# Performance work log

Hardware: AMD Instinct MI355X
Metric: run time of the kernel (lower is better)

Reference implementation:

```python
import jax, jax.numpy as jnp
import numpy as np

HIDDEN = 1024
NUM_HEADS = 16
HEAD_DIM = HIDDEN // NUM_HEADS  # 64
ROPE_DIM = HEAD_DIM // 2        # 32 (per-axis rotary dim)
EPS = 1e-6


def _make_rope_tables(dim, grid_h, grid_w, theta=10000.0):
    # pt_seq_len == ft_seq_len, so t_h = arange(H), t_w = arange(W)
    freqs = 1.0 / theta ** (np.arange(0, dim, 2, dtype=np.float32)[: dim // 2] / dim)  # [dim//2]
    fh = np.repeat(np.outer(np.arange(grid_h, dtype=np.float32), freqs), 2, axis=-1)  # [H, dim]
    fw = np.repeat(np.outer(np.arange(grid_w, dtype=np.float32), freqs), 2, axis=-1)  # [W, dim]
    fh = np.broadcast_to(fh[:, None, :], (grid_h, grid_w, dim))
    fw = np.broadcast_to(fw[None, :, :], (grid_h, grid_w, dim))
    f2d = np.concatenate([fh, fw], axis=-1).reshape(grid_h * grid_w, 2 * dim)  # [HW, 2*dim]
    return jnp.asarray(np.cos(f2d)), jnp.asarray(np.sin(f2d))


def _rms_norm(x, w, eps=EPS):
    var = jnp.mean(jnp.square(x), axis=-1, keepdims=True)
    return x * jax.lax.rsqrt(var + eps) * w


def _rotate_half(x):
    x1 = x[..., 0::2]
    x2 = x[..., 1::2]
    return jnp.stack([-x2, x1], axis=-1).reshape(x.shape)


def _apply_rope(x, cos, sin):
    # x: [B, H, S, D]; cos/sin: [S, D]
    return x * cos + _rotate_half(x) * sin


def setup_inputs() -> dict:
    key = jax.random.key(0)
    ks = jax.random.split(key, 12)
    B, IMG_H, IMG_W, CND_H, CND_W = 2, 64, 64, 32, 32
    img_len, cnd_len = IMG_H * IMG_W, CND_H * CND_W
    xav = (6.0 / (HIDDEN + HIDDEN)) ** 0.5
    inp = {
        'image_tokens': jax.random.normal(ks[0], (B, img_len, HIDDEN), jnp.float32),
        'condition_tokens': jax.random.normal(ks[1], (B, cnd_len, HIDDEN), jnp.float32),
        'q_norm_w': jnp.ones((HIDDEN,), jnp.float32),
        'kv_norm_w': jnp.ones((HIDDEN,), jnp.float32),
        'q_head_norm_w': jnp.ones((HEAD_DIM,), jnp.float32),
        'k_head_norm_w': jnp.ones((HEAD_DIM,), jnp.float32),
        'q_w': jax.random.uniform(ks[2], (HIDDEN, HIDDEN), jnp.float32, -xav, xav),
        'q_b': jnp.zeros((HIDDEN,), jnp.float32),
        'k_w': jax.random.uniform(ks[3], (HIDDEN, HIDDEN), jnp.float32, -xav, xav),
        'k_b': jnp.zeros((HIDDEN,), jnp.float32),
        'v_w': jax.random.uniform(ks[4], (HIDDEN, HIDDEN), jnp.float32, -xav, xav),
        'v_b': jnp.zeros((HIDDEN,), jnp.float32),
        'o_w': jax.random.uniform(ks[5], (HIDDEN, HIDDEN), jnp.float32, -xav, xav),
        'o_b': jnp.zeros((HIDDEN,), jnp.float32),
        'alpha': jnp.full((1,), 0.5, jnp.float32),  # nonzero so backward exercises the attn path
    }
    ic, isn = _make_rope_tables(ROPE_DIM, IMG_H, IMG_W)
    cc, cs = _make_rope_tables(ROPE_DIM, CND_H, CND_W)
    inp.update(image_cos=ic, image_sin=isn, cond_cos=cc, cond_sin=cs)
    return inp


def reference(image_tokens, condition_tokens, q_norm_w, kv_norm_w, q_head_norm_w,
              k_head_norm_w, q_w, q_b, k_w, k_b, v_w, v_b, o_w, o_b, alpha,
              image_cos, image_sin, cond_cos, cond_sin):
    B, Li, _ = image_tokens.shape
    Lc = condition_tokens.shape[1]
    qn = _rms_norm(image_tokens, q_norm_w)
    kvn = _rms_norm(condition_tokens, kv_norm_w)
    # projections (torch Linear: x @ W.T + b); weights here stored [out, in]
    q = (qn @ q_w.T + q_b).reshape(B, Li, NUM_HEADS, HEAD_DIM).transpose(0, 2, 1, 3)
    k = (kvn @ k_w.T + k_b).reshape(B, Lc, NUM_HEADS, HEAD_DIM).transpose(0, 2, 1, 3)
    v = (kvn @ v_w.T + v_b).reshape(B, Lc, NUM_HEADS, HEAD_DIM).transpose(0, 2, 1, 3)
    q = _rms_norm(q, q_head_norm_w)
    k = _rms_norm(k, k_head_norm_w)
    q = _apply_rope(q, image_cos, image_sin)
    k = _apply_rope(k, cond_cos, cond_sin)
    scale = 1.0 / jnp.sqrt(jnp.asarray(HEAD_DIM, q.dtype))
    scores = jnp.einsum('bhqd,bhkd->bhqk', q, k) * scale
    attn = jax.nn.softmax(scores, axis=-1)
    out = jnp.einsum('bhqk,bhkd->bhqd', attn, v)
    out = out.transpose(0, 2, 1, 3).reshape(B, Li, HIDDEN)
    update = out @ o_w.T + o_b
    return image_tokens + alpha.reshape(1, 1, 1) * update
```

## Files before the change

kernel.cpp:

```cpp
#include <hip/hip_runtime.h>

typedef __bf16 bf16x8 __attribute__((ext_vector_type(8)));
typedef __bf16 bf16x4 __attribute__((ext_vector_type(4)));
typedef float  f32x4  __attribute__((ext_vector_type(4)));
typedef float  f32x16 __attribute__((ext_vector_type(16)));
typedef unsigned u32x2 __attribute__((ext_vector_type(2)));

#define DEVINL __device__ __forceinline__

DEVINL void gload_lds16(const void* g, void* l) {
  __builtin_amdgcn_global_load_lds((const __attribute__((address_space(1))) void*)g,
                                   (__attribute__((address_space(3))) void*)l, 16, 0, 0);
}

DEVINL unsigned pkbf(float a, float b) {
  union { __bf16 h[2]; unsigned u; } c;
  c.h[0] = (__bf16)a; c.h[1] = (__bf16)b;
  return c.u;
}

DEVINL float fast_exp2(float x) {
#if __has_builtin(__builtin_amdgcn_exp2f)
  return __builtin_amdgcn_exp2f(x);
#else
  float r;
  asm volatile("v_exp_f32 %0, %1" : "=v"(r) : "v"(x));
  return r;
#endif
}

DEVINL float2 swap32(float x) {
  u32x2 r = __builtin_amdgcn_permlane32_swap(__float_as_uint(x), __float_as_uint(x), false, false);
  return make_float2(__uint_as_float(r.x), __uint_as_float(r.y));
}

__global__ __launch_bounds__(256) void prep_kernel(
    const float* __restrict__ XA, const float* __restrict__ WA, __bf16* __restrict__ YA,
    const float* __restrict__ XB, const float* __restrict__ WB, __bf16* __restrict__ YB,
    const float* __restrict__ wq, const float* __restrict__ wk,
    const float* __restrict__ wv, const float* __restrict__ wo,
    __bf16* __restrict__ oq, __bf16* __restrict__ ok,
    __bf16* __restrict__ ov, __bf16* __restrict__ oo) {
  int rb = blockIdx.x, tid = threadIdx.x;
  if (rb < 10240) {
    const float* X; const float* W; __bf16* Y; int row;
    if (rb < 8192) { X = XA; W = WA; Y = YA; row = rb; }
    else { X = XB; W = WB; Y = YB; row = rb - 8192; }
    const float4* xr = (const float4*)(X + (size_t)row * 1024);
    float4 v = xr[tid];
    float ss = v.x * v.x + v.y * v.y + v.z * v.z + v.w * v.w;
#pragma unroll
    for (int m = 1; m < 64; m <<= 1) ss += __shfl_xor(ss, m);
    __shared__ float part[4];
    if ((tid & 63) == 0) part[tid >> 6] = ss;
    __syncthreads();
    float tot = part[0] + part[1] + part[2] + part[3];
    float rn = rsqrtf(tot * (1.0f / 1024.0f) + 1e-6f);
    float4 wv4 = ((const float4*)W)[tid];
    bf16x4 y;
    y[0] = (__bf16)(v.x * rn * wv4.x);
    y[1] = (__bf16)(v.y * rn * wv4.y);
    y[2] = (__bf16)(v.z * rn * wv4.z);
    y[3] = (__bf16)(v.w * rn * wv4.w);
    *(bf16x4*)(Y + (size_t)row * 1024 + tid * 4) = y;
  } else {
    int gid = (rb - 10240) * 256 + tid;
    int which = gid >> 17;
    size_t off = (size_t)(gid & 131071) * 8;
    const float* s = (which == 0) ? wq : (which == 1) ? wk : (which == 2) ? wv : wo;
    __bf16* o = (which == 0) ? oq : (which == 1) ? ok : (which == 2) ? ov : oo;
    float4 v0 = *(const float4*)(s + off), v1 = *(const float4*)(s + off + 4);
    bf16x8 y;
    y[0] = (__bf16)v0.x; y[1] = (__bf16)v0.y; y[2] = (__bf16)v0.z; y[3] = (__bf16)v0.w;
    y[4] = (__bf16)v1.x; y[5] = (__bf16)v1.y; y[6] = (__bf16)v1.z; y[7] = (__bf16)v1.w;
    *(bf16x8*)(o + off) = y;
  }
}

template <typename EPIF>
DEVINL void gemm_core(const __bf16* __restrict__ A, const __bf16* __restrict__ Bw,
                      int m0, int n0, char* AsB, char* BsB, EPIF epi) {
  int tid = threadIdx.x, lane = tid & 63, w = tid >> 6, wr = w >> 1, wc = w & 1;
  f32x4 z4 = {0.f, 0.f, 0.f, 0.f};
  f32x4 acc[4][4];
#pragma unroll
  for (int i = 0; i < 4; i++)
#pragma unroll
    for (int j = 0; j < 4; j++) acc[i][j] = z4;

  auto STAGE = [&](int k0, int bsel) {
#pragma unroll
    for (int i = 0; i < 2; i++) {
      int chunk = i * 256 + tid;
      int row = chunk >> 2, cc = chunk & 3;
      gload_lds16(A + (size_t)(m0 + row) * 1024 + k0 + cc * 8,
                  AsB + bsel * 8192 + i * 4096 + w * 1024);
      gload_lds16(Bw + (size_t)(n0 + row) * 1024 + k0 + cc * 8,
                  BsB + bsel * 8192 + i * 4096 + w * 1024);
    }
  };

  STAGE(0, 0);
  int b = 0;
  for (int it = 0; it < 32; ++it) {
    if (it < 31) {
      STAGE((it + 1) * 32, b ^ 1);
      asm volatile("s_waitcnt vmcnt(4)" ::: "memory");
    } else {
      asm volatile("s_waitcnt vmcnt(0)" ::: "memory");
    }
    __builtin_amdgcn_s_barrier();
    asm volatile("" ::: "memory");
    const char* As = AsB + b * 8192;
    const char* Bs = BsB + b * 8192;
    bf16x8 af[4], bfr[4];
#pragma unroll
    for (int m = 0; m < 4; m++) {
      int r = wr * 64 + m * 16 + (lane & 15);
      af[m] = *(const bf16x8*)(As + r * 64 + ((lane >> 4) << 4));
    }
#pragma unroll
    for (int n = 0; n < 4; n++) {
      int r = wc * 64 + n * 16 + (lane & 15);
      bfr[n] = *(const bf16x8*)(Bs + r * 64 + ((lane >> 4) << 4));
    }
    __builtin_amdgcn_s_setprio(1);
#pragma unroll
    for (int m = 0; m < 4; m++)
#pragma unroll
      for (int n = 0; n < 4; n++)
        acc[m][n] = __builtin_amdgcn_mfma_f32_16x16x32_bf16(af[m], bfr[n], acc[m][n], 0, 0, 0);
    __builtin_amdgcn_s_setprio(0);
    __builtin_amdgcn_s_barrier();
    asm volatile("" ::: "memory");
    b ^= 1;
  }
  epi(acc, lane, wr, wc);
}

__global__ __launch_bounds__(256) void qkv_gemm_kernel(
    const __bf16* __restrict__ qn, const __bf16* __restrict__ kvn,
    const __bf16* __restrict__ wq, const __bf16* __restrict__ wkv,
    const float* __restrict__ qb, const float* __restrict__ kb, const float* __restrict__ vb,
    __bf16* __restrict__ Qt, __bf16* __restrict__ Kt, __bf16* __restrict__ Vt0) {
  __shared__ __attribute__((aligned(16))) char AsB[2 * 8192];
  __shared__ __attribute__((aligned(16))) char BsB[2 * 8192];
  int id = blockIdx.x;
  const __bf16 *A, *Bw; const float* bias; __bf16* Cout;
  int m0, n0, nloc;
  if (id < 512) {
    A = qn; Bw = wq; m0 = (id & 63) * 128; n0 = (id >> 6) * 128; nloc = n0;
    bias = qb; Cout = Qt;
  } else {
    int i2 = id - 512;
    A = kvn; Bw = wkv; m0 = (i2 & 15) * 128; n0 = (i2 >> 4) * 128;
    if (n0 < 1024) { bias = kb; Cout = Kt; nloc = n0; }
    else { bias = vb; Cout = Vt0; nloc = n0 - 1024; }
  }
  gemm_core(A, Bw, m0, n0, AsB, BsB,
            [&](f32x4 (&acc)[4][4], int lane, int wr, int wc) {
#pragma unroll
              for (int m = 0; m < 4; m++)
#pragma unroll
                for (int n = 0; n < 4; n++) {
                  int col = nloc + wc * 64 + n * 16 + (lane & 15);
                  float bv = bias[col];
#pragma unroll
                  for (int r = 0; r < 4; r++) {
                    int row = m0 + wr * 64 + m * 16 + ((lane >> 4) << 2) + r;
                    Cout[((size_t)row << 10) + col] = (__bf16)(acc[m][n][r] + bv);
                  }
                }
            });
}

__global__ __launch_bounds__(256) void gemm_o_kernel(
    const __bf16* __restrict__ A, const __bf16* __restrict__ Bw,
    const float* __restrict__ bias, float* __restrict__ Cout,
    const float* __restrict__ resid, const float* __restrict__ alphap) {
  __shared__ __attribute__((aligned(16))) char AsB[2 * 8192];
  __shared__ __attribute__((aligned(16))) char BsB[2 * 8192];
  int m0 = blockIdx.x * 128, n0 = blockIdx.y * 128;
  float aval = alphap[0];
  gemm_core(A, Bw, m0, n0, AsB, BsB,
            [&](f32x4 (&acc)[4][4], int lane, int wr, int wc) {
#pragma unroll
              for (int m = 0; m < 4; m++)
#pragma unroll
                for (int n = 0; n < 4; n++) {
                  int col = n0 + wc * 64 + n * 16 + (lane & 15);
                  float bv = bias[col];
#pragma unroll
                  for (int r = 0; r < 4; r++) {
                    int row = m0 + wr * 64 + m * 16 + ((lane >> 4) << 2) + r;
                    size_t idx = ((size_t)row << 10) + col;
                    Cout[idx] = resid[idx] + aval * (acc[m][n][r] + bv);
                  }
                }
            });
}

__global__ __launch_bounds__(256) void kprep_kernel(
    const __bf16* __restrict__ Kt, const float* __restrict__ KHW,
    const float* __restrict__ CCOS, const float* __restrict__ CSIN,
    __bf16* __restrict__ Kr,
    const __bf16* __restrict__ V, __bf16* __restrict__ Vt) {
  int rb = blockIdx.x, tid = threadIdx.x;
  if (rb < 1024) {
    int inst = rb * 32 + (tid >> 3);
    int sub = tid & 7;
    int token = inst >> 4, h = inst & 15;
    int b = token >> 10, pos = token & 1023;
    const __bf16* xp = Kt + ((size_t)token << 10) + h * 64 + sub * 8;
    bf16x8 xv = *(const bf16x8*)xp;
    float xf[8];
#pragma unroll
    for (int i = 0; i < 8; i++) xf[i] = (float)xv[i];
    float ss = 0.f;
#pragma unroll
    for (int i = 0; i < 8; i++) ss += xf[i] * xf[i];
    ss += __shfl_xor(ss, 1);
    ss += __shfl_xor(ss, 2);
    ss += __shfl_xor(ss, 4);
    float rn = rsqrtf(ss * (1.0f / 64.0f) + 1e-6f);
    const float* hwp = KHW + sub * 8;
    const float* cp = CCOS + ((size_t)pos << 6) + sub * 8;
    const float* sp = CSIN + ((size_t)pos << 6) + sub * 8;
    float xn[8], o[8];
#pragma unroll
    for (int i = 0; i < 8; i++) xn[i] = xf[i] * rn * hwp[i];
#pragma unroll
    for (int i = 0; i < 8; i += 2) {
      o[i] = xn[i] * cp[i] - xn[i + 1] * sp[i];
      o[i + 1] = xn[i + 1] * cp[i + 1] + xn[i] * sp[i + 1];
    }
    bf16x8 yv;
#pragma unroll
    for (int i = 0; i < 8; i++) yv[i] = (__bf16)o[i];
    *(bf16x8*)(Kr + (((size_t)((b << 4) + h) << 10) + pos) * 64 + sub * 8) = yv;
  } else {
    int bx = rb - 1024;
    int bh = bx >> 4;
    int j0 = (bx & 15) * 64;
    int b = bh >> 4, h = bh & 15;
#pragma unroll
    for (int it = 0; it < 2; ++it) {
      int c = it * 256 + tid;
      int jl = c >> 3, d0 = (c & 7) * 8;
      bf16x8 v = *(const bf16x8*)(V + (size_t)(b * 1024 + j0 + jl) * 1024 + h * 64 + d0);
#pragma unroll
      for (int i = 0; i < 8; i++)
        Vt[((size_t)bh * 64 + d0 + i) * 1024 + j0 + jl] = v[i];
    }
  }
}

__global__ __launch_bounds__(256, 3) void attn_kernel(
    const __bf16* __restrict__ Qt, const float* __restrict__ QHW,
    const float* __restrict__ QCOS, const float* __restrict__ QSIN,
    const __bf16* __restrict__ Kr, const __bf16* __restrict__ Vtr,
    __bf16* __restrict__ AO) {
  int tid = threadIdx.x, lane = tid & 63, w = tid >> 6;
  int lq = lane & 31, hi = lane >> 5;
  int wgid = blockIdx.x;
  int nid = (wgid & 7) * 128 + (wgid >> 3);
  int q0 = (nid & 31) * 128;
  int bh = nid >> 5, b = bh >> 4, h = bh & 15;
  const float QSC = 0.125f * 1.44269504088896340736f;

  __shared__ __attribute__((aligned(16))) __bf16 Ks[2][4096];
  __shared__ __attribute__((aligned(16))) __bf16 Vs[2][4096];

  const __bf16* Kbh = Kr + ((size_t)bh << 16);
  const __bf16* Vbh = Vtr + ((size_t)bh << 16);

  auto STAGE = [&](int T, int BSEL) {
#pragma unroll
    for (int i = 0; i < 2; i++) {
      int s = 2 * w + i;
      int kt = s >> 2, ds2 = s & 3;
      gload_lds16(Kbh + (size_t)(T * 64 + kt * 32 + lq) * 64 + ds2 * 16 + hi * 8,
                  (char*)Ks[BSEL] + s * 1024);
      int f = s >> 1, dh = s & 1;
      gload_lds16(Vbh + (size_t)(dh * 32 + lq) * 1024 + T * 64 + f * 16 + hi * 8,
                  (char*)Vs[BSEL] + s * 1024);
    }
  };

  STAGE(0, 0);

  bf16x8 qf[4];
  {
    int pos = q0 + w * 32 + lq;
    const __bf16* qp = Qt + ((size_t)(b * 4096 + pos) << 10) + h * 64 + hi * 8;
    float xf[4][8];
    float ss = 0.f;
#pragma unroll
    for (int ds = 0; ds < 4; ds++) {
      bf16x8 xv = *(const bf16x8*)(qp + ds * 16);
#pragma unroll
      for (int j = 0; j < 8; j++) { float f = (float)xv[j]; xf[ds][j] = f; ss += f * f; }
    }
    float2 sw = swap32(ss);
    float rn = rsqrtf((sw.x + sw.y) * (1.0f / 64.0f) + 1e-6f);
#pragma unroll
    for (int ds = 0; ds < 4; ds++) {
      int d0 = ds * 16 + hi * 8;
      const float* wp = QHW + d0;
      const float* cp = QCOS + ((size_t)pos << 6) + d0;
      const float* sp = QSIN + ((size_t)pos << 6) + d0;
      float4 wa = *(const float4*)wp, wb = *(const float4*)(wp + 4);
      float4 ca = *(const float4*)cp, cb = *(const float4*)(cp + 4);
      float4 sa = *(const float4*)sp, sb = *(const float4*)(sp + 4);
      float wv[8] = {wa.x, wa.y, wa.z, wa.w, wb.x, wb.y, wb.z, wb.w};
      float cv[8] = {ca.x, ca.y, ca.z, ca.w, cb.x, cb.y, cb.z, cb.w};
      float sv[8] = {sa.x, sa.y, sa.z, sa.w, sb.x, sb.y, sb.z, sb.w};
      float xn[8];
#pragma unroll
      for (int j = 0; j < 8; j++) xn[j] = xf[ds][j] * rn * wv[j];
      bf16x8 q8;
#pragma unroll
      for (int j = 0; j < 8; j += 2) {
        q8[j]     = (__bf16)((xn[j] * cv[j] - xn[j + 1] * sv[j]) * QSC);
        q8[j + 1] = (__bf16)((xn[j + 1] * cv[j + 1] + xn[j] * sv[j + 1]) * QSC);
      }
      qf[ds] = q8;
    }
  }

  f32x16 Z16;
#pragma unroll
  for (int r = 0; r < 16; r++) Z16[r] = 0.f;
  f32x16 accO[2];
  accO[0] = Z16; accO[1] = Z16;
  float srun = 0.f;

  int buf = 0;
  for (int t = 0; t < 16; t++) {
    if (t < 15) {
      STAGE(t + 1, buf ^ 1);
      asm volatile("s_waitcnt vmcnt(4)" ::: "memory");
    } else {
      asm volatile("s_waitcnt vmcnt(0)" ::: "memory");
    }
    __builtin_amdgcn_s_barrier();
    asm volatile("" ::: "memory");

    const char* kbase = (const char*)Ks[buf];
    const char* vbase = (const char*)Vs[buf];
    int loff = lane * 16;

    bf16x8 kf[8];
#pragma unroll
    for (int s = 0; s < 8; s++) kf[s] = *(const bf16x8*)(kbase + s * 1024 + loff);

    f32x16 accS[2];
    __builtin_amdgcn_s_setprio(1);
#pragma unroll
    for (int kt = 0; kt < 2; kt++) {
      accS[kt] = __builtin_amdgcn_mfma_f32_32x32x16_bf16(kf[kt * 4], qf[0], Z16, 0, 0, 0);
#pragma unroll
      for (int ds = 1; ds < 4; ds++)
        accS[kt] = __builtin_amdgcn_mfma_f32_32x32x16_bf16(kf[kt * 4 + ds], qf[ds], accS[kt], 0, 0, 0);
    }
    __builtin_amdgcn_s_setprio(0);

    float ssum = 0.f;
#pragma unroll
    for (int kt = 0; kt < 2; kt++)
#pragma unroll
      for (int r = 0; r < 16; r++) {
        float e = fast_exp2(accS[kt][r]);
        accS[kt][r] = e;
        ssum += e;
      }
    float2 sws = swap32(ssum);
    srun += sws.x + sws.y;

    unsigned pa[4][4];
#pragma unroll
    for (int kt = 0; kt < 2; kt++)
#pragma unroll
      for (int s2 = 0; s2 < 2; s2++) {
        int f = kt * 2 + s2, rb = s2 * 8;
        unsigned u  = pkbf(accS[kt][rb + 0], accS[kt][rb + 1]);
        unsigned v2 = pkbf(accS[kt][rb + 2], accS[kt][rb + 3]);
        unsigned w2 = pkbf(accS[kt][rb + 4], accS[kt][rb + 5]);
        unsigned x2 = pkbf(accS[kt][rb + 6], accS[kt][rb + 7]);
        u32x2 r02 = __builtin_amdgcn_permlane32_swap(u, w2, false, false);
        u32x2 r13 = __builtin_amdgcn_permlane32_swap(v2, x2, false, false);
        pa[f][0] = r02.x; pa[f][1] = r13.x; pa[f][2] = r02.y; pa[f][3] = r13.y;
      }

    bf16x8 vf[8];
#pragma unroll
    for (int s = 0; s < 8; s++) vf[s] = *(const bf16x8*)(vbase + s * 1024 + loff);

    __builtin_amdgcn_s_setprio(1);
#pragma unroll
    for (int f = 0; f < 4; f++) {
      union { unsigned u[4]; bf16x8 v; } pf;
      pf.u[0] = pa[f][0]; pf.u[1] = pa[f][1]; pf.u[2] = pa[f][2]; pf.u[3] = pa[f][3];
#pragma unroll
      for (int dh = 0; dh < 2; dh++)
        accO[dh] = __builtin_amdgcn_mfma_f32_32x32x16_bf16(pf.v, vf[f * 2 + dh], accO[dh], 0, 0, 0);
    }
    __builtin_amdgcn_s_setprio(0);

    __builtin_amdgcn_s_barrier();
    asm volatile("" ::: "memory");
    buf ^= 1;
  }

  __bf16* aobase = AO + (((size_t)b * 4096) << 10) + h * 64;
  float rinv = 1.0f / srun;
  int ri = __float_as_int(rinv);
#pragma unroll
  for (int r = 0; r < 16; r++) {
    int cr = (r & 3) + ((r >> 2) << 3) + (hi << 2);
    float rv = __int_as_float(__builtin_amdgcn_ds_bpermute(cr << 2, ri));
    size_t rowoff = ((size_t)(q0 + w * 32 + cr) << 10);
#pragma unroll
    for (int dh = 0; dh < 2; dh++)
      aobase[rowoff + dh * 32 + lq] = (__bf16)(accO[dh][r] * rv);
  }
}

extern "C" void kernel_launch(void* const* d_in, const int* in_sizes, int n_in,
                              void* d_out, int out_size, void* d_ws, size_t ws_size,
                              hipStream_t stream) {
  const float* img  = (const float*)d_in[0];
  const float* cnd  = (const float*)d_in[1];
  const float* qnw  = (const float*)d_in[2];
  const float* kvnw = (const float*)d_in[3];
  const float* qhw  = (const float*)d_in[4];
  const float* khw  = (const float*)d_in[5];
  const float* qw   = (const float*)d_in[6];
  const float* qb   = (const float*)d_in[7];
  const float* kw   = (const float*)d_in[8];
  const float* kb   = (const float*)d_in[9];
  const float* vw   = (const float*)d_in[10];
  const float* vb   = (const float*)d_in[11];
  const float* ow   = (const float*)d_in[12];
  const float* ob   = (const float*)d_in[13];
  const float* alpha= (const float*)d_in[14];
  const float* icos = (const float*)d_in[15];
  const float* isin = (const float*)d_in[16];
  const float* ccos = (const float*)d_in[17];
  const float* csin = (const float*)d_in[18];
  float* out = (float*)d_out;

  __bf16* p = (__bf16*)d_ws;
  __bf16* wqb = p; p += 1048576;
  __bf16* wkb = p; p += 1048576;
  __bf16* wvb = p; p += 1048576;
  __bf16* wob = p; p += 1048576;
  __bf16* qn  = p; p += 8388608;
  __bf16* kvn = p; p += 2097152;
  __bf16* Qt  = p; p += 8388608;
  __bf16* Kt  = p; p += 2097152;
  __bf16* Vt0 = p; p += 2097152;
  __bf16* Kr  = p; p += 2097152;
  __bf16* Vtr = p; p += 2097152;
  __bf16* AO  = qn;

  prep_kernel<<<12288, 256, 0, stream>>>(img, qnw, qn, cnd, kvnw, kvn,
                                         qw, kw, vw, ow, wqb, wkb, wvb, wob);

  qkv_gemm_kernel<<<768, 256, 0, stream>>>(qn, kvn, wqb, wkb, qb, kb, vb, Qt, Kt, Vt0);

  kprep_kernel<<<1536, 256, 0, stream>>>(Kt, khw, ccos, csin, Kr, Vt0, Vtr);

  attn_kernel<<<1024, 256, 0, stream>>>(Qt, qhw, icos, isin, Kr, Vtr, AO);

  gemm_o_kernel<<<dim3(64, 8), 256, 0, stream>>>(AO, wob, ob, out, img, alpha);
}
```

Baseline: 152.0 us.

## Split QK tiles into halves to cut registers and raise attention occupancy

Raises the attention kernel's launch bound from 3 to 4 waves per SIMD. The QK^T compute now runs in two 32-key halves that reuse one accumulator, so the exp/pack of one half overlaps with the MFMAs of the next and fewer registers are live at once. Staging addresses are precomputed once outside the loop, which removes per-iteration address arithmetic. The tighter register budget could cause spills, and the compiler's reordering may not give the intended overlap.

```diff
diff --git a/kernel.cpp b/kernel.cpp
--- a/kernel.cpp
+++ b/kernel.cpp
@@ -255,7 +255,7 @@
   }
 }
 
-__global__ __launch_bounds__(256, 3) void attn_kernel(
+__global__ __launch_bounds__(256, 4) void attn_kernel(
     const __bf16* __restrict__ Qt, const float* __restrict__ QHW,
     const float* __restrict__ QCOS, const float* __restrict__ QSIN,
     const __bf16* __restrict__ Kr, const __bf16* __restrict__ Vtr,
@@ -271,20 +271,17 @@
   __shared__ __attribute__((aligned(16))) __bf16 Ks[2][4096];
   __shared__ __attribute__((aligned(16))) __bf16 Vs[2][4096];
 
-  const __bf16* Kbh = Kr + ((size_t)bh << 16);
-  const __bf16* Vbh = Vtr + ((size_t)bh << 16);
+  int s0 = 2 * w, s1 = 2 * w + 1;
+  const __bf16* kSrc0 = Kr + ((size_t)bh << 16) + (size_t)((s0 >> 2) * 32 + lq) * 64 + (s0 & 3) * 16 + hi * 8;
+  const __bf16* kSrc1 = Kr + ((size_t)bh << 16) + (size_t)((s1 >> 2) * 32 + lq) * 64 + (s1 & 3) * 16 + hi * 8;
+  const __bf16* vSrc0 = Vtr + ((size_t)bh << 16) + (size_t)((s0 & 1) * 32 + lq) * 1024 + (s0 >> 1) * 16 + hi * 8;
+  const __bf16* vSrc1 = Vtr + ((size_t)bh << 16) + (size_t)((s1 & 1) * 32 + lq) * 1024 + (s1 >> 1) * 16 + hi * 8;
 
   auto STAGE = [&](int T, int BSEL) {
-#pragma unroll
-    for (int i = 0; i < 2; i++) {
-      int s = 2 * w + i;
-      int kt = s >> 2, ds2 = s & 3;
-      gload_lds16(Kbh + (size_t)(T * 64 + kt * 32 + lq) * 64 + ds2 * 16 + hi * 8,
-                  (char*)Ks[BSEL] + s * 1024);
-      int f = s >> 1, dh = s & 1;
-      gload_lds16(Vbh + (size_t)(dh * 32 + lq) * 1024 + T * 64 + f * 16 + hi * 8,
-                  (char*)Vs[BSEL] + s * 1024);
-    }
+    gload_lds16(kSrc0 + (size_t)T * 4096, (char*)Ks[BSEL] + s0 * 1024);
+    gload_lds16(kSrc1 + (size_t)T * 4096, (char*)Ks[BSEL] + s1 * 1024);
+    gload_lds16(vSrc0 + T * 64, (char*)Vs[BSEL] + s0 * 1024);
+    gload_lds16(vSrc1 + T * 64, (char*)Vs[BSEL] + s1 * 1024);
   };
 
   STAGE(0, 0);
@@ -334,6 +331,7 @@
   f32x16 accO[2];
   accO[0] = Z16; accO[1] = Z16;
   float srun = 0.f;
+  int loff = lane * 16;
 
   int buf = 0;
   for (int t = 0; t < 16; t++) {
@@ -348,53 +346,74 @@
 
     const char* kbase = (const char*)Ks[buf];
     const char* vbase = (const char*)Vs[buf];
-    int loff = lane * 16;
-
-    bf16x8 kf[8];
-#pragma unroll
-    for (int s = 0; s < 8; s++) kf[s] = *(const bf16x8*)(kbase + s * 1024 + loff);
-
-    f32x16 accS[2];
+
+    unsigned pa[4][4];
+    float ssum = 0.f;
+
+    bf16x8 kfA[4];
+#pragma unroll
+    for (int s = 0; s < 4; s++) kfA[s] = *(const bf16x8*)(kbase + s * 1024 + loff);
+    f32x16 accS;
     __builtin_amdgcn_s_setprio(1);
-#pragma unroll
-    for (int kt = 0; kt < 2; kt++) {
-      accS[kt] = __builtin_amdgcn_mfma_f32_32x32x16_bf16(kf[kt * 4], qf[0], Z16, 0, 0, 0);
-#pragma unroll
-      for (int ds = 1; ds < 4; ds++)
-        accS[kt] = __builtin_amdgcn_mfma_f32_32x32x16_bf16(kf[kt * 4 + ds], qf[ds], accS[kt], 0, 0, 0);
-    }
+    accS = __builtin_amdgcn_mfma_f32_32x32x16_bf16(kfA[0], qf[0], Z16, 0, 0, 0);
+#pragma unroll
+    for (int ds = 1; ds < 4; ds++)
+      accS = __builtin_amdgcn_mfma_f32_32x32x16_bf16(kfA[ds], qf[ds], accS, 0, 0, 0);
     __builtin_amdgcn_s_setprio(0);
 
-    float ssum = 0.f;
-#pragma unroll
-    for (int kt = 0; kt < 2; kt++)
-#pragma unroll
-      for (int r = 0; r < 16; r++) {
-        float e = fast_exp2(accS[kt][r]);
-        accS[kt][r] = e;
-        ssum += e;
-      }
+    bf16x8 kfB[4];
+#pragma unroll
+    for (int s = 0; s < 4; s++) kfB[s] = *(const bf16x8*)(kbase + (4 + s) * 1024 + loff);
+
+#pragma unroll
+    for (int r = 0; r < 16; r++) {
+      float e = fast_exp2(accS[r]);
+      accS[r] = e;
+      ssum += e;
+    }
+#pragma unroll
+    for (int s2 = 0; s2 < 2; s2++) {
+      int rb = s2 * 8;
+      unsigned u  = pkbf(accS[rb + 0], accS[rb + 1]);
+      unsigned v2 = pkbf(accS[rb + 2], accS[rb + 3]);
+      unsigned w2 = pkbf(accS[rb + 4], accS[rb + 5]);
+      unsigned x2 = pkbf(accS[rb + 6], accS[rb + 7]);
+      u32x2 r02 = __builtin_amdgcn_permlane32_swap(u, w2, false, false);
+      u32x2 r13 = __builtin_amdgcn_permlane32_swap(v2, x2, false, false);
+      pa[s2][0] = r02.x; pa[s2][1] = r13.x; pa[s2][2] = r02.y; pa[s2][3] = r13.y;
+    }
+
+    __builtin_amdgcn_s_setprio(1);
+    accS = __builtin_amdgcn_mfma_f32_32x32x16_bf16(kfB[0], qf[0], Z16, 0, 0, 0);
+#pragma unroll
+    for (int ds = 1; ds < 4; ds++)
+      accS = __builtin_amdgcn_mfma_f32_32x32x16_bf16(kfB[ds], qf[ds], accS, 0, 0, 0);
+    __builtin_amdgcn_s_setprio(0);
+
+    bf16x8 vf[8];
+#pragma unroll
+    for (int s = 0; s < 8; s++) vf[s] = *(const bf16x8*)(vbase + s * 1024 + loff);
+
+#pragma unroll
+    for (int r = 0; r < 16; r++) {
+      float e = fast_exp2(accS[r]);
+      accS[r] = e;
+      ssum += e;
+    }
+#pragma unroll
+    for (int s2 = 0; s2 < 2; s2++) {
+      int rb = s2 * 8;
+      unsigned u  = pkbf(accS[rb + 0], accS[rb + 1]);
+      unsigned v2 = pkbf(accS[rb + 2], accS[rb + 3]);
+      unsigned w2 = pkbf(accS[rb + 4], accS[rb + 5]);
+      unsigned x2 = pkbf(accS[rb + 6], accS[rb + 7]);
+      u32x2 r02 = __builtin_amdgcn_permlane32_swap(u, w2, false, false);
+      u32x2 r13 = __builtin_amdgcn_permlane32_swap(v2, x2, false, false);
+      pa[2 + s2][0] = r02.x; pa[2 + s2][1] = r13.x; pa[2 + s2][2] = r02.y; pa[2 + s2][3] = r13.y;
+    }
+
     float2 sws = swap32(ssum);
     srun += sws.x + sws.y;
-
-    unsigned pa[4][4];
-#pragma unroll
-    for (int kt = 0; kt < 2; kt++)
-#pragma unroll
-      for (int s2 = 0; s2 < 2; s2++) {
-        int f = kt * 2 + s2, rb = s2 * 8;
-        unsigned u  = pkbf(accS[kt][rb + 0], accS[kt][rb + 1]);
-        unsigned v2 = pkbf(accS[kt][rb + 2], accS[kt][rb + 3]);
-        unsigned w2 = pkbf(accS[kt][rb + 4], accS[kt][rb + 5]);
-        unsigned x2 = pkbf(accS[kt][rb + 6], accS[kt][rb + 7]);
-        u32x2 r02 = __builtin_amdgcn_permlane32_swap(u, w2, false, false);
-        u32x2 r13 = __builtin_amdgcn_permlane32_swap(v2, x2, false, false);
-        pa[f][0] = r02.x; pa[f][1] = r13.x; pa[f][2] = r02.y; pa[f][3] = r13.y;
-      }
-
-    bf16x8 vf[8];
-#pragma unroll
-    for (int s = 0; s < 8; s++) vf[s] = *(const bf16x8*)(vbase + s * 1024 + loff);
 
     __builtin_amdgcn_s_setprio(1);
 #pragma unroll
```

New measurement: 152.3 us. About the same (+0.2%).

## Triple-buffer GEMM and attention, two query tiles per wave, bit-trick exp

Applied to the files above, without the earlier changes.

The shared GEMM core and the attention kernel move from double to triple buffering of LDS tiles, with the next-but-one stage issued after the fragment reads. Each attention wave now processes two 32-row query tiles, so every staged K/V tile is reused twice and the grid is halved. Softmax exp2 is replaced by a Schraudolph-style fma plus truncation that produces bf16 bits directly. Row sums are accumulated by an extra MFMA against a ones vector and inverted with a hardware reciprocal. The trade-offs are more LDS and register pressure (occupancy hint lowered from 3 to 2 blocks) and a coarser exponential approximation.

```diff
diff --git a/kernel.cpp b/kernel.cpp
--- a/kernel.cpp
+++ b/kernel.cpp
@@ -13,25 +13,17 @@
                                    (__attribute__((address_space(3))) void*)l, 16, 0, 0);
 }
 
-DEVINL unsigned pkbf(float a, float b) {
-  union { __bf16 h[2]; unsigned u; } c;
-  c.h[0] = (__bf16)a; c.h[1] = (__bf16)b;
-  return c.u;
-}
-
-DEVINL float fast_exp2(float x) {
-#if __has_builtin(__builtin_amdgcn_exp2f)
-  return __builtin_amdgcn_exp2f(x);
-#else
-  float r;
-  asm volatile("v_exp_f32 %0, %1" : "=v"(r) : "v"(x));
-  return r;
-#endif
-}
-
 DEVINL float2 swap32(float x) {
   u32x2 r = __builtin_amdgcn_permlane32_swap(__float_as_uint(x), __float_as_uint(x), false, false);
   return make_float2(__uint_as_float(r.x), __uint_as_float(r.y));
+}
+
+DEVINL float fast_rcp(float x) {
+#if __has_builtin(__builtin_amdgcn_rcpf)
+  return __builtin_amdgcn_rcpf(x);
+#else
+  return 1.0f / x;
+#endif
 }
 
 __global__ __launch_bounds__(256) void prep_kernel(
@@ -101,18 +93,15 @@
   };
 
   STAGE(0, 0);
-  int b = 0;
+  STAGE(32, 1);
+  asm volatile("s_waitcnt vmcnt(4)" ::: "memory");
+  __builtin_amdgcn_s_barrier();
+  asm volatile("" ::: "memory");
+
   for (int it = 0; it < 32; ++it) {
-    if (it < 31) {
-      STAGE((it + 1) * 32, b ^ 1);
-      asm volatile("s_waitcnt vmcnt(4)" ::: "memory");
-    } else {
-      asm volatile("s_waitcnt vmcnt(0)" ::: "memory");
-    }
-    __builtin_amdgcn_s_barrier();
-    asm volatile("" ::: "memory");
-    const char* As = AsB + b * 8192;
-    const char* Bs = BsB + b * 8192;
+    int bsel = it % 3;
+    const char* As = AsB + bsel * 8192;
+    const char* Bs = BsB + bsel * 8192;
     bf16x8 af[4], bfr[4];
 #pragma unroll
     for (int m = 0; m < 4; m++) {
@@ -124,6 +113,7 @@
       int r = wc * 64 + n * 16 + (lane & 15);
       bfr[n] = *(const bf16x8*)(Bs + r * 64 + ((lane >> 4) << 4));
     }
+    if (it + 2 < 32) STAGE((it + 2) * 32, (it + 2) % 3);
     __builtin_amdgcn_s_setprio(1);
 #pragma unroll
     for (int m = 0; m < 4; m++)
@@ -131,9 +121,13 @@
       for (int n = 0; n < 4; n++)
         acc[m][n] = __builtin_amdgcn_mfma_f32_16x16x32_bf16(af[m], bfr[n], acc[m][n], 0, 0, 0);
     __builtin_amdgcn_s_setprio(0);
+    if (it + 2 < 32) {
+      asm volatile("s_waitcnt vmcnt(4)" ::: "memory");
+    } else if (it + 1 < 32) {
+      asm volatile("s_waitcnt vmcnt(0)" ::: "memory");
+    }
     __builtin_amdgcn_s_barrier();
     asm volatile("" ::: "memory");
-    b ^= 1;
   }
   epi(acc, lane, wr, wc);
 }
@@ -143,8 +137,8 @@
     const __bf16* __restrict__ wq, const __bf16* __restrict__ wkv,
     const float* __restrict__ qb, const float* __restrict__ kb, const float* __restrict__ vb,
     __bf16* __restrict__ Qt, __bf16* __restrict__ Kt, __bf16* __restrict__ Vt0) {
-  __shared__ __attribute__((aligned(16))) char AsB[2 * 8192];
-  __shared__ __attribute__((aligned(16))) char BsB[2 * 8192];
+  __shared__ __attribute__((aligned(16))) char AsB[3 * 8192];
+  __shared__ __attribute__((aligned(16))) char BsB[3 * 8192];
   int id = blockIdx.x;
   const __bf16 *A, *Bw; const float* bias; __bf16* Cout;
   int m0, n0, nloc;
@@ -178,8 +172,8 @@
     const __bf16* __restrict__ A, const __bf16* __restrict__ Bw,
     const float* __restrict__ bias, float* __restrict__ Cout,
     const float* __restrict__ resid, const float* __restrict__ alphap) {
-  __shared__ __attribute__((aligned(16))) char AsB[2 * 8192];
-  __shared__ __attribute__((aligned(16))) char BsB[2 * 8192];
+  __shared__ __attribute__((aligned(16))) char AsB[3 * 8192];
+  __shared__ __attribute__((aligned(16))) char BsB[3 * 8192];
   int m0 = blockIdx.x * 128, n0 = blockIdx.y * 128;
   float aval = alphap[0];
   gemm_core(A, Bw, m0, n0, AsB, BsB,
@@ -255,7 +249,7 @@
   }
 }
 
-__global__ __launch_bounds__(256, 3) void attn_kernel(
+__global__ __launch_bounds__(256, 2) void attn_kernel(
     const __bf16* __restrict__ Qt, const float* __restrict__ QHW,
     const float* __restrict__ QCOS, const float* __restrict__ QSIN,
     const __bf16* __restrict__ Kr, const __bf16* __restrict__ Vtr,
@@ -263,13 +257,14 @@
   int tid = threadIdx.x, lane = tid & 63, w = tid >> 6;
   int lq = lane & 31, hi = lane >> 5;
   int wgid = blockIdx.x;
-  int nid = (wgid & 7) * 128 + (wgid >> 3);
-  int q0 = (nid & 31) * 128;
-  int bh = nid >> 5, b = bh >> 4, h = bh & 15;
+  int nid = (wgid & 7) * 64 + (wgid >> 3);
+  int q0 = (nid & 15) * 256;
+  int bh = nid >> 4, b = bh >> 4, h = bh & 15;
   const float QSC = 0.125f * 1.44269504088896340736f;
-
-  __shared__ __attribute__((aligned(16))) __bf16 Ks[2][4096];
-  __shared__ __attribute__((aligned(16))) __bf16 Vs[2][4096];
+  const float MAGIC = 16250.5f;
+
+  __shared__ __attribute__((aligned(16))) __bf16 Ks[3][4096];
+  __shared__ __attribute__((aligned(16))) __bf16 Vs[3][4096];
 
   const __bf16* Kbh = Kr + ((size_t)bh << 16);
   const __bf16* Vbh = Vtr + ((size_t)bh << 16);
@@ -288,10 +283,12 @@
   };
 
   STAGE(0, 0);
-
-  bf16x8 qf[4];
-  {
-    int pos = q0 + w * 32 + lq;
+  STAGE(1, 1);
+
+  bf16x8 qf[2][4];
+#pragma unroll
+  for (int qt = 0; qt < 2; qt++) {
+    int pos = q0 + w * 64 + qt * 32 + lq;
     const __bf16* qp = Qt + ((size_t)(b * 4096 + pos) << 10) + h * 64 + hi * 8;
     float xf[4][8];
     float ss = 0.f;
@@ -324,105 +321,109 @@
         q8[j]     = (__bf16)((xn[j] * cv[j] - xn[j + 1] * sv[j]) * QSC);
         q8[j + 1] = (__bf16)((xn[j + 1] * cv[j + 1] + xn[j] * sv[j + 1]) * QSC);
       }
-      qf[ds] = q8;
+      qf[qt][ds] = q8;
     }
   }
 
   f32x16 Z16;
 #pragma unroll
   for (int r = 0; r < 16; r++) Z16[r] = 0.f;
-  f32x16 accO[2];
-  accO[0] = Z16; accO[1] = Z16;
-  float srun = 0.f;
-
-  int buf = 0;
+  f32x16 accO[2][2];
+  f32x16 accR[2];
+#pragma unroll
+  for (int qt = 0; qt < 2; qt++) {
+    accO[qt][0] = Z16; accO[qt][1] = Z16; accR[qt] = Z16;
+  }
+  bf16x8 ones8;
+#pragma unroll
+  for (int i = 0; i < 8; i++) ones8[i] = (__bf16)1.0f;
+
+  asm volatile("s_waitcnt vmcnt(4)" ::: "memory");
+  __builtin_amdgcn_s_barrier();
+  asm volatile("" ::: "memory");
+
   for (int t = 0; t < 16; t++) {
-    if (t < 15) {
-      STAGE(t + 1, buf ^ 1);
+    int cur = t % 3;
+    const char* kbase = (const char*)Ks[cur];
+    const char* vbase = (const char*)Vs[cur];
+    int loff = lane * 16;
+
+    bf16x8 kf[8], vf[8];
+#pragma unroll
+    for (int s = 0; s < 8; s++) kf[s] = *(const bf16x8*)(kbase + s * 1024 + loff);
+#pragma unroll
+    for (int s = 0; s < 8; s++) vf[s] = *(const bf16x8*)(vbase + s * 1024 + loff);
+
+    if (t + 2 < 16) STAGE(t + 2, (t + 2) % 3);
+
+    f32x16 accS[2][2];
+    __builtin_amdgcn_s_setprio(1);
+#pragma unroll
+    for (int qt = 0; qt < 2; qt++)
+#pragma unroll
+      for (int kt = 0; kt < 2; kt++) {
+        accS[qt][kt] = __builtin_amdgcn_mfma_f32_32x32x16_bf16(kf[kt * 4], qf[qt][0], Z16, 0, 0, 0);
+#pragma unroll
+        for (int ds = 1; ds < 4; ds++)
+          accS[qt][kt] = __builtin_amdgcn_mfma_f32_32x32x16_bf16(kf[kt * 4 + ds], qf[qt][ds], accS[qt][kt], 0, 0, 0);
+      }
+    __builtin_amdgcn_s_setprio(0);
+
+    unsigned pa[2][4][4];
+#pragma unroll
+    for (int qt = 0; qt < 2; qt++)
+#pragma unroll
+      for (int kt = 0; kt < 2; kt++)
+#pragma unroll
+        for (int s2 = 0; s2 < 2; s2++) {
+          int f = kt * 2 + s2, rb = s2 * 8;
+          unsigned q[4];
+#pragma unroll
+          for (int i = 0; i < 4; i++) {
+            float t0 = fmaf(accS[qt][kt][rb + 2 * i], 128.f, MAGIC);
+            float t1 = fmaf(accS[qt][kt][rb + 2 * i + 1], 128.f, MAGIC);
+            q[i] = ((unsigned)t1 << 16) | (unsigned)t0;
+          }
+          u32x2 r02 = __builtin_amdgcn_permlane32_swap(q[0], q[2], false, false);
+          u32x2 r13 = __builtin_amdgcn_permlane32_swap(q[1], q[3], false, false);
+          pa[qt][f][0] = r02.x; pa[qt][f][1] = r13.x; pa[qt][f][2] = r02.y; pa[qt][f][3] = r13.y;
+        }
+
+    __builtin_amdgcn_s_setprio(1);
+#pragma unroll
+    for (int f = 0; f < 4; f++)
+#pragma unroll
+      for (int qt = 0; qt < 2; qt++) {
+        union { unsigned u[4]; bf16x8 v; } pf;
+        pf.u[0] = pa[qt][f][0]; pf.u[1] = pa[qt][f][1];
+        pf.u[2] = pa[qt][f][2]; pf.u[3] = pa[qt][f][3];
+        accO[qt][0] = __builtin_amdgcn_mfma_f32_32x32x16_bf16(pf.v, vf[f * 2 + 0], accO[qt][0], 0, 0, 0);
+        accO[qt][1] = __builtin_amdgcn_mfma_f32_32x32x16_bf16(pf.v, vf[f * 2 + 1], accO[qt][1], 0, 0, 0);
+        accR[qt]    = __builtin_amdgcn_mfma_f32_32x32x16_bf16(pf.v, ones8, accR[qt], 0, 0, 0);
+      }
+    __builtin_amdgcn_s_setprio(0);
+
+    if (t + 2 < 16) {
       asm volatile("s_waitcnt vmcnt(4)" ::: "memory");
-    } else {
+    } else if (t + 1 < 16) {
       asm volatile("s_waitcnt vmcnt(0)" ::: "memory");
     }
     __builtin_amdgcn_s_barrier();
     asm volatile("" ::: "memory");
-
-    const char* kbase = (const char*)Ks[buf];
-    const char* vbase = (const char*)Vs[buf];
-    int loff = lane * 16;
-
-    bf16x8 kf[8];
-#pragma unroll
-    for (int s = 0; s < 8; s++) kf[s] = *(const bf16x8*)(kbase + s * 1024 + loff);
-
-    f32x16 accS[2];
-    __builtin_amdgcn_s_setprio(1);
-#pragma unroll
-    for (int kt = 0; kt < 2; kt++) {
-      accS[kt] = __builtin_amdgcn_mfma_f32_32x32x16_bf16(kf[kt * 4], qf[0], Z16, 0, 0, 0);
-#pragma unroll
-      for (int ds = 1; ds < 4; ds++)
-        accS[kt] = __builtin_amdgcn_mfma_f32_32x32x16_bf16(kf[kt * 4 + ds], qf[ds], accS[kt], 0, 0, 0);
-    }
-    __builtin_amdgcn_s_setprio(0);
-
-    float ssum = 0.f;
-#pragma unroll
-    for (int kt = 0; kt < 2; kt++)
-#pragma unroll
-      for (int r = 0; r < 16; r++) {
-        float e = fast_exp2(accS[kt][r]);
-        accS[kt][r] = e;
-        ssum += e;
-      }
-    float2 sws = swap32(ssum);
-    srun += sws.x + sws.y;
-
-    unsigned pa[4][4];
-#pragma unroll
-    for (int kt = 0; kt < 2; kt++)
-#pragma unroll
-      for (int s2 = 0; s2 < 2; s2++) {
-        int f = kt * 2 + s2, rb = s2 * 8;
-        unsigned u  = pkbf(accS[kt][rb + 0], accS[kt][rb + 1]);
-        unsigned v2 = pkbf(accS[kt][rb + 2], accS[kt][rb + 3]);
-        unsigned w2 = pkbf(accS[kt][rb + 4], accS[kt][rb + 5]);
-        unsigned x2 = pkbf(accS[kt][rb + 6], accS[kt][rb + 7]);
-        u32x2 r02 = __builtin_amdgcn_permlane32_swap(u, w2, false, false);
-        u32x2 r13 = __builtin_amdgcn_permlane32_swap(v2, x2, false, false);
-        pa[f][0] = r02.x; pa[f][1] = r13.x; pa[f][2] = r02.y; pa[f][3] = r13.y;
-      }
-
-    bf16x8 vf[8];
-#pragma unroll
-    for (int s = 0; s < 8; s++) vf[s] = *(const bf16x8*)(vbase + s * 1024 + loff);
-
-    __builtin_amdgcn_s_setprio(1);
-#pragma unroll
-    for (int f = 0; f < 4; f++) {
-      union { unsigned u[4]; bf16x8 v; } pf;
-      pf.u[0] = pa[f][0]; pf.u[1] = pa[f][1]; pf.u[2] = pa[f][2]; pf.u[3] = pa[f][3];
+  }
+
+  __bf16* aobase = AO + (((size_t)b * 4096) << 10) + h * 64;
+#pragma unroll
+  for (int qt = 0; qt < 2; qt++) {
+#pragma unroll
+    for (int r = 0; r < 16; r++) {
+      float rv = fast_rcp(accR[qt][r]);
+      int cr = (r & 3) + ((r >> 2) << 3) + (hi << 2);
+      size_t rowoff = ((size_t)(q0 + w * 64 + qt * 32 + cr) << 10);
 #pragma unroll
       for (int dh = 0; dh < 2; dh++)
-        accO[dh] = __builtin_amdgcn_mfma_f32_32x32x16_bf16(pf.v, vf[f * 2 + dh], accO[dh], 0, 0, 0);
-    }
-    __builtin_amdgcn_s_setprio(0);
-
-    __builtin_amdgcn_s_barrier();
-    asm volatile("" ::: "memory");
-    buf ^= 1;
-  }
-
-  __bf16* aobase = AO + (((size_t)b * 4096) << 10) + h * 64;
-  float rinv = 1.0f / srun;
-  int ri = __float_as_int(rinv);
-#pragma unroll
-  for (int r = 0; r < 16; r++) {
-    int cr = (r & 3) + ((r >> 2) << 3) + (hi << 2);
-    float rv = __int_as_float(__builtin_amdgcn_ds_bpermute(cr << 2, ri));
-    size_t rowoff = ((size_t)(q0 + w * 32 + cr) << 10);
-#pragma unroll
-    for (int dh = 0; dh < 2; dh++)
-      aobase[rowoff + dh * 32 + lq] = (__bf16)(accO[dh][r] * rv);
+        aobase[rowoff + dh * 32 + lq] = (__bf16)(accO[qt][dh][r] * rv);
+    }
   }
 }
 
@@ -471,7 +472,7 @@
 
   kprep_kernel<<<1536, 256, 0, stream>>>(Kt, khw, ccos, csin, Kr, Vt0, Vtr);
 
-  attn_kernel<<<1024, 256, 0, stream>>>(Qt, qhw, icos, isin, Kr, Vtr, AO);
+  attn_kernel<<<512, 256, 0, stream>>>(Qt, qhw, icos, isin, Kr, Vtr, AO);
 
   gemm_o_kernel<<<dim3(64, 8), 256, 0, stream>>>(AO, wob, ob, out, img, alpha);
 }
```

Result: faster. 133.7 us (-12.0%).
